# Kernel optimization log

Measured on AMD Instinct MI355X. Metric: run time of the kernel, lower is better.

Reference implementation:

```python
import jax, jax.numpy as jnp
import numpy as np

N_NODES = 10000
N_EDGES = 320000
F = 128
N_RBF = 20


def setup_inputs() -> dict:
    key = jax.random.key(0)
    ks = jax.random.split(key, 12)
    inp = {
        "idx_i": jax.random.randint(ks[0], (N_EDGES,), 0, N_NODES),
        "idx_j": jax.random.randint(ks[1], (N_EDGES,), 0, N_NODES),
        "rel_dir": jax.random.normal(ks[2], (N_EDGES, 3), dtype=jnp.float32),
        "rel_dist_cut": jax.random.uniform(ks[3], (N_EDGES,), dtype=jnp.float32),
        "rbf_features": jax.random.normal(ks[4], (N_EDGES, N_RBF), dtype=jnp.float32),
        "scalar_features": jax.random.normal(ks[5], (N_NODES, F), dtype=jnp.float32),
        "vector_features": jax.random.normal(ks[6], (N_NODES, F, 3), dtype=jnp.float32),
        # learned params: scalar_network = Linear(F,F) -> SiLU -> Linear(F,3F); rbf_network = Linear(N_RBF,3F)
        "W1": jax.random.normal(ks[7], (F, F), dtype=jnp.float32) / np.sqrt(F),
        "b1": jnp.zeros((F,), dtype=jnp.float32),
        "W2": jax.random.normal(ks[8], (F, 3 * F), dtype=jnp.float32) / np.sqrt(F),
        "b2": jnp.zeros((3 * F,), dtype=jnp.float32),
        "Wr": jax.random.normal(ks[9], (N_RBF, 3 * F), dtype=jnp.float32) / np.sqrt(N_RBF),
        "br": jnp.zeros((3 * F,), dtype=jnp.float32),
    }
    return inp


def reference(idx_i, idx_j, rel_dir, rel_dist_cut, rbf_features,
              scalar_features, vector_features, W1, b1, W2, b2, Wr, br):
    num_nodes, num_features = scalar_features.shape
    # per-node MLP: [N, 3F]
    phi = jax.nn.silu(scalar_features @ W1 + b1) @ W2 + b2
    # distance gate: [E, 3F]
    Wg = (rbf_features @ Wr + br) * rel_dist_cut[:, None]
    # gather neighbor phi and gate
    phi_W = phi[idx_j] * Wg                       # [E, 3F]
    phi_W_vv = phi_W[:, :num_features]            # [E, F]
    phi_W_ss = phi_W[:, num_features:2 * num_features]
    phi_W_vs = phi_W[:, 2 * num_features:]
    # per-receiver edge counts (bincount)
    counts = jax.ops.segment_sum(jnp.ones((idx_i.shape[0],), phi_W.dtype),
                                 idx_i, num_segments=num_nodes)  # [N]
    scalar_residuals = jax.ops.segment_sum(phi_W_ss, idx_i, num_segments=num_nodes)
    scalar_residuals = scalar_residuals / counts[:, None]
    # per-edge vector message: [E, F, 3]
    v_edge = (vector_features[idx_j] * phi_W_vv[:, :, None]
              + phi_W_vs[:, :, None] * rel_dir[:, None, :])
    vector_residuals = jax.ops.segment_sum(v_edge, idx_i, num_segments=num_nodes)
    vector_residuals = vector_residuals / counts[:, None, None]
    return (scalar_features + scalar_residuals,
            vector_features + vector_residuals)
```

## Files before the change

### kernel.cpp

```cpp
#include <hip/hip_runtime.h>
#include <hip/hip_bf16.h>

#define NN 10000
#define NE 320000
#define FDIM 128
#define NRBF 20
#define PHI_DIM 384
#define NKEY NN
#define SCAN_BLOCKS 40

typedef unsigned int uint;
typedef unsigned short ushort;

#if __has_builtin(__builtin_amdgcn_fdot2_f32_bf16)
#define USE_DOT2 1
typedef __bf16 bf16x2 __attribute__((ext_vector_type(2)));
#else
#define USE_DOT2 0
#endif

__device__ __forceinline__ ushort f2bf(float x) {
  __hip_bfloat16 b = __float2bfloat16(x);
  return *(ushort*)&b;
}


__global__ void phi_kernel(const float* __restrict__ S, const float* __restrict__ W1,
                           const float* __restrict__ b1, const float* __restrict__ W2,
                           const float* __restrict__ b2, const float* __restrict__ vf,
                           const int* __restrict__ idx_i, int* __restrict__ counts,
                           char* __restrict__ tab) {
  __shared__ float s_s[8][FDIM];
  __shared__ float h_s[8][FDIM];
  const int t = threadIdx.x;
  const int n0 = blockIdx.x * 8;
  {
    const int e0 = (blockIdx.x * 128 + t) * 2;
    atomicAdd(&counts[idx_i[e0]], 1);
    atomicAdd(&counts[idx_i[e0 + 1]], 1);
  }
  ushort vz[8];
#pragma unroll
  for (int n = 0; n < 8; n++) {
    const int node = n0 + n;
    const float* src = vf + (size_t)node * (FDIM * 3) + t * 3;
    char* pb = tab + (size_t)node * 1536;
    ((uint*)(pb + 1024))[t] = ((uint)f2bf(src[1]) << 16) | f2bf(src[0]);
    vz[n] = f2bf(src[2]);
  }
#pragma unroll
  for (int n = 0; n < 8; n++) s_s[n][t] = S[(n0 + n) * FDIM + t];
  __syncthreads();
  float acc[8];
#pragma unroll
  for (int n = 0; n < 8; n++) acc[n] = 0.f;
  for (int k = 0; k < FDIM; k++) {
    float w = W1[k * FDIM + t];
#pragma unroll
    for (int n = 0; n < 8; n++) acc[n] += s_s[n][k] * w;
  }
  float bb = b1[t];
#pragma unroll
  for (int n = 0; n < 8; n++) {
    float x = acc[n] + bb;
    h_s[n][t] = x / (1.0f + expf(-x));
  }
  __syncthreads();
  float a0[8], a1[8], a2[8];
#pragma unroll
  for (int n = 0; n < 8; n++) { a0[n] = 0.f; a1[n] = 0.f; a2[n] = 0.f; }
  for (int k = 0; k < FDIM; k++) {
    float w0 = W2[k * PHI_DIM + t];
    float w1 = W2[k * PHI_DIM + t + 128];
    float w2 = W2[k * PHI_DIM + t + 256];
#pragma unroll
    for (int n = 0; n < 8; n++) {
      float hv = h_s[n][k];
      a0[n] += hv * w0;
      a1[n] += hv * w1;
      a2[n] += hv * w2;
    }
  }
  float c0 = b2[t], c1 = b2[t + 128], c2 = b2[t + 256];
#pragma unroll
  for (int n = 0; n < 8; n++) {
    char* pb = tab + (size_t)(n0 + n) * 1536;
    ((uint*)pb)[t] = ((uint)f2bf(a1[n] + c1) << 16) | f2bf(a0[n] + c0);
    ((uint*)(pb + 512))[t] = ((uint)vz[n] << 16) | f2bf(a2[n] + c2);
  }
}

__global__ void scan1_kernel(const int* __restrict__ counts, int* __restrict__ offsets,
                             int* __restrict__ blocksums) {
  __shared__ int s[256];
  const int t = threadIdx.x;
  const int idx = blockIdx.x * 256 + t;
  const int c = counts[idx];
  s[t] = c;
  __syncthreads();
  for (int off = 1; off < 256; off <<= 1) {
    int v = (t >= off) ? s[t - off] : 0;
    __syncthreads();
    s[t] += v;
    __syncthreads();
  }
  if (idx < NKEY) offsets[idx] = s[t] - c;
  if (t == 255) blocksums[blockIdx.x] = s[255];
}

__global__ void scan2_kernel(int* __restrict__ blocksums, int* __restrict__ offsets) {
  __shared__ int s[64];
  const int t = threadIdx.x;
  int v0 = (t < SCAN_BLOCKS) ? blocksums[t] : 0;
  s[t] = v0;
  __syncthreads();
  for (int off = 1; off < 64; off <<= 1) {
    int v = (t >= off) ? s[t - off] : 0;
    __syncthreads();
    s[t] += v;
    __syncthreads();
  }
  if (t < SCAN_BLOCKS) blocksums[t] = s[t] - v0;
  if (t == SCAN_BLOCKS - 1) offsets[NKEY] = s[t];
}

__global__ void scan3_kernel(int* __restrict__ offsets, const int* __restrict__ blocksums) {
  const int idx = blockIdx.x * 256 + threadIdx.x;
  if (idx < NKEY) offsets[idx] += blocksums[blockIdx.x];
}

__global__ void stage_kernel(const int* __restrict__ idx_i, const int* __restrict__ idx_j,
                             const float* __restrict__ cut, const float* __restrict__ dir,
                             const float* __restrict__ rbf, const int* __restrict__ offsets,
                             int* __restrict__ cursor, uint* __restrict__ edata,
                             int* __restrict__ jlist) {
  int e = blockIdx.x * blockDim.x + threadIdx.x;
  if (e >= NE) return;
  int i = idx_i[e];
  int pos = atomicAdd(&cursor[i], 1);
  const int slot = offsets[i] + pos;
  const int j = idx_j[e];
  jlist[slot] = j;
  uint* d = edata + (size_t)slot * 16;
  const float c = cut[e];
  d[0] = (uint)j;
  d[1] = __float_as_uint(c);
  d[2] = __float_as_uint(dir[e * 3 + 0]);
  d[3] = __float_as_uint(dir[e * 3 + 1]);
  d[4] = __float_as_uint(dir[e * 3 + 2]);
  d[5] = 0u;
  const float* rb = rbf + (size_t)e * NRBF;
#pragma unroll
  for (int r = 0; r < 10; r++) {
    uint lo = (uint)f2bf(rb[2 * r] * c);
    uint hi = (uint)f2bf(rb[2 * r + 1] * c);
    d[6 + r] = (hi << 16) | lo;
  }
}

__global__ __launch_bounds__(128, 5) void node_kernel(
    const uint* __restrict__ edata, const int* __restrict__ jlist,
    const float* __restrict__ Wr, const float* __restrict__ br,
    const char* __restrict__ tab, const float* __restrict__ sf,
    const float* __restrict__ vf, const int* __restrict__ offsets,
    float* __restrict__ out) {
  const int f = threadIdx.x;
#if USE_DOT2
  bf16x2 wrA[10], wrB[10], wrC[10];
#pragma unroll
  for (int r = 0; r < 10; r++) {
    uint a = ((uint)f2bf(Wr[(2 * r + 1) * PHI_DIM + f]) << 16) | f2bf(Wr[(2 * r) * PHI_DIM + f]);
    uint b = ((uint)f2bf(Wr[(2 * r + 1) * PHI_DIM + f + 128]) << 16) |
             f2bf(Wr[(2 * r) * PHI_DIM + f + 128]);
    uint c = ((uint)f2bf(Wr[(2 * r + 1) * PHI_DIM + f + 256]) << 16) |
             f2bf(Wr[(2 * r) * PHI_DIM + f + 256]);
    wrA[r] = __builtin_bit_cast(bf16x2, a);
    wrB[r] = __builtin_bit_cast(bf16x2, b);
    wrC[r] = __builtin_bit_cast(bf16x2, c);
  }
#else
  float wrA[NRBF], wrB[NRBF], wrC[NRBF];
#pragma unroll
  for (int r = 0; r < NRBF; r++) {
    wrA[r] = Wr[r * PHI_DIM + f];
    wrB[r] = Wr[r * PHI_DIM + f + 128];
    wrC[r] = Wr[r * PHI_DIM + f + 256];
  }
#endif
  const int n = blockIdx.x;
  const int beg = offsets[n], end = offsets[n + 1];
  const float br0 = br[f], br1 = br[f + 128], br2 = br[f + 256];
  float ss = 0.f, ax = 0.f, ay = 0.f, az = 0.f;
  const int f4 = f * 4;

  auto process = [&](const uint4* rec, uint pq, uint zq, uint vq) {
    uint4 q0 = rec[0];
    uint4 q1 = rec[1];
    uint4 q2 = rec[2];
    uint4 q3 = rec[3];
    const float c = __uint_as_float(q0.y);
    const float dx = __uint_as_float(q0.z);
    const float dy = __uint_as_float(q0.w);
    const float dz = __uint_as_float(q1.x);
    uint rbp[10] = {q1.z, q1.w, q2.x, q2.y, q2.z, q2.w, q3.x, q3.y, q3.z, q3.w};
    float g0 = 0.f, g1 = 0.f, g2 = 0.f;
#if USE_DOT2
#pragma unroll
    for (int r = 0; r < 10; r++) {
      bf16x2 rp = __builtin_bit_cast(bf16x2, rbp[r]);
      g0 = __builtin_amdgcn_fdot2_f32_bf16(rp, wrA[r], g0, false);
      g1 = __builtin_amdgcn_fdot2_f32_bf16(rp, wrB[r], g1, false);
      g2 = __builtin_amdgcn_fdot2_f32_bf16(rp, wrC[r], g2, false);
    }
#else
#pragma unroll
    for (int r = 0; r < 10; r++) {
      float rlo = __uint_as_float(rbp[r] << 16);
      float rhi = __uint_as_float(rbp[r] & 0xffff0000u);
      g0 += rlo * wrA[2 * r] + rhi * wrA[2 * r + 1];
      g1 += rlo * wrB[2 * r] + rhi * wrB[2 * r + 1];
      g2 += rlo * wrC[2 * r] + rhi * wrC[2 * r + 1];
    }
#endif
    g0 += br0 * c;
    g1 += br1 * c;
    g2 += br2 * c;
    const float vv = __uint_as_float(pq << 16) * g0;
    const float sv = __uint_as_float(pq & 0xffff0000u) * g1;
    const float vs = __uint_as_float(zq << 16) * g2;
    ss += sv;
    ax += __uint_as_float(vq << 16) * vv + vs * dx;
    ay += __uint_as_float(vq & 0xffff0000u) * vv + vs * dy;
    az += __uint_as_float(zq & 0xffff0000u) * vv + vs * dz;
  };

  int p = beg;
  for (; p + 2 <= end; p += 2) {
    const int j0 = jlist[p];
    const int j1 = jlist[p + 1];
    const char* B0 = tab + (size_t)j0 * 1536;
    const char* B1 = tab + (size_t)j1 * 1536;
    const uint pq0 = *(const uint*)(B0 + f4);
    const uint zq0 = *(const uint*)(B0 + 512 + f4);
    const uint vq0 = *(const uint*)(B0 + 1024 + f4);
    const uint pq1 = *(const uint*)(B1 + f4);
    const uint zq1 = *(const uint*)(B1 + 512 + f4);
    const uint vq1 = *(const uint*)(B1 + 1024 + f4);
    const uint4* r0 = (const uint4*)(edata + (size_t)p * 16);
    const uint4* r1 = (const uint4*)(edata + (size_t)(p + 1) * 16);
    process(r0, pq0, zq0, vq0);
    process(r1, pq1, zq1, vq1);
  }
  if (p < end) {
    const int j0 = jlist[p];
    const char* B0 = tab + (size_t)j0 * 1536;
    const uint pq0 = *(const uint*)(B0 + f4);
    const uint zq0 = *(const uint*)(B0 + 512 + f4);
    const uint vq0 = *(const uint*)(B0 + 1024 + f4);
    process((const uint4*)(edata + (size_t)p * 16), pq0, zq0, vq0);
  }

  const float inv = 1.0f / (float)(end - beg);
  out[(size_t)n * FDIM + f] = sf[(size_t)n * FDIM + f] + ss * inv;
  float* ov = out + (size_t)NN * FDIM + (size_t)n * (FDIM * 3) + f * 3;
  const float* iv = vf + (size_t)n * (FDIM * 3) + f * 3;
  ov[0] = iv[0] + ax * inv;
  ov[1] = iv[1] + ay * inv;
  ov[2] = iv[2] + az * inv;
}

extern "C" void kernel_launch(void* const* d_in, const int* in_sizes, int n_in,
                              void* d_out, int out_size, void* d_ws, size_t ws_size,
                              hipStream_t stream) {
  const int* idx_i = (const int*)d_in[0];
  const int* idx_j = (const int*)d_in[1];
  const float* rel_dir = (const float*)d_in[2];
  const float* cut = (const float*)d_in[3];
  const float* rbf = (const float*)d_in[4];
  const float* sf = (const float*)d_in[5];
  const float* vf = (const float*)d_in[6];
  const float* W1 = (const float*)d_in[7];
  const float* b1 = (const float*)d_in[8];
  const float* W2 = (const float*)d_in[9];
  const float* b2 = (const float*)d_in[10];
  const float* Wr = (const float*)d_in[11];
  const float* br = (const float*)d_in[12];
  float* out = (float*)d_out;

  char* w = (char*)d_ws;
  int* counts = (int*)w;
  int* cursor = (int*)(w + 40960);
  int* offsets = (int*)(w + 81920);
  int* blocksums = (int*)(w + 122944);
  uint* edata = (uint*)(w + 123200);
  char* tab = w + 20603200;
  int* jlist = (int*)(w + 35963200);

  hipMemsetAsync(w, 0, 81920, stream);
  hipLaunchKernelGGL(phi_kernel, dim3(NN / 8), dim3(128), 0, stream, sf, W1, b1, W2, b2, vf,
                     idx_i, counts, tab);
  hipLaunchKernelGGL(scan1_kernel, dim3(SCAN_BLOCKS), dim3(256), 0, stream, counts, offsets,
                     blocksums);
  hipLaunchKernelGGL(scan2_kernel, dim3(1), dim3(64), 0, stream, blocksums, offsets);
  hipLaunchKernelGGL(scan3_kernel, dim3(SCAN_BLOCKS), dim3(256), 0, stream, offsets, blocksums);
  hipLaunchKernelGGL(stage_kernel, dim3((NE + 255) / 256), dim3(256), 0, stream, idx_i, idx_j,
                     cut, rel_dir, rbf, offsets, cursor, edata, jlist);
  hipLaunchKernelGGL(node_kernel, dim3(NN), dim3(128), 0, stream, edata, jlist, Wr, br, tab, sf,
                     vf, offsets, out);
}
```

Before: 165.6 us.

## Premultiply neighbor vectors by phi_vv per node and shrink gather table

The per-node table now stores vector_features times phi_vv (in bf16) instead of phi_vv and the raw vectors separately. This moves the multiply from the edge loop to the node kernel and shrinks each node's row from 1536 to 1280 bytes, cutting gather traffic in node_kernel. The stage kernel reuses the counts array as a decrementing cursor, which removes the separate cursor buffer and its memset. Rounding to bf16 now happens after the product rather than on each factor, which slightly changes numerics.

```diff
diff --git a/kernel.cpp b/kernel.cpp
--- a/kernel.cpp
+++ b/kernel.cpp
@@ -39,15 +39,6 @@
     atomicAdd(&counts[idx_i[e0]], 1);
     atomicAdd(&counts[idx_i[e0 + 1]], 1);
   }
-  ushort vz[8];
-#pragma unroll
-  for (int n = 0; n < 8; n++) {
-    const int node = n0 + n;
-    const float* src = vf + (size_t)node * (FDIM * 3) + t * 3;
-    char* pb = tab + (size_t)node * 1536;
-    ((uint*)(pb + 1024))[t] = ((uint)f2bf(src[1]) << 16) | f2bf(src[0]);
-    vz[n] = f2bf(src[2]);
-  }
 #pragma unroll
   for (int n = 0; n < 8; n++) s_s[n][t] = S[(n0 + n) * FDIM + t];
   __syncthreads();
@@ -84,9 +75,18 @@
   float c0 = b2[t], c1 = b2[t + 128], c2 = b2[t + 256];
 #pragma unroll
   for (int n = 0; n < 8; n++) {
-    char* pb = tab + (size_t)(n0 + n) * 1536;
-    ((uint*)pb)[t] = ((uint)f2bf(a1[n] + c1) << 16) | f2bf(a0[n] + c0);
-    ((uint*)(pb + 512))[t] = ((uint)vz[n] << 16) | f2bf(a2[n] + c2);
+    const int node = n0 + n;
+    const float p0 = a0[n] + c0;
+    const float p1 = a1[n] + c1;
+    const float p2 = a2[n] + c2;
+    const float* src = vf + (size_t)node * (FDIM * 3) + t * 3;
+    const uint wx = f2bf(src[0] * p0);
+    const uint wy = f2bf(src[1] * p0);
+    const uint wz = f2bf(src[2] * p0);
+    char* pb = tab + (size_t)node * 1280;
+    ((uint*)pb)[t] = (wy << 16) | wx;
+    ((uint*)(pb + 512))[t] = ((uint)f2bf(p1) << 16) | wz;
+    ((ushort*)(pb + 1024))[t] = f2bf(p2);
   }
 }
 
@@ -132,12 +132,12 @@
 __global__ void stage_kernel(const int* __restrict__ idx_i, const int* __restrict__ idx_j,
                              const float* __restrict__ cut, const float* __restrict__ dir,
                              const float* __restrict__ rbf, const int* __restrict__ offsets,
-                             int* __restrict__ cursor, uint* __restrict__ edata,
+                             int* __restrict__ counts, uint* __restrict__ edata,
                              int* __restrict__ jlist) {
   int e = blockIdx.x * blockDim.x + threadIdx.x;
   if (e >= NE) return;
   int i = idx_i[e];
-  int pos = atomicAdd(&cursor[i], 1);
+  int pos = atomicSub(&counts[i], 1) - 1;
   const int slot = offsets[i] + pos;
   const int j = idx_j[e];
   jlist[slot] = j;
@@ -193,7 +193,7 @@
   float ss = 0.f, ax = 0.f, ay = 0.f, az = 0.f;
   const int f4 = f * 4;
 
-  auto process = [&](const uint4* rec, uint pq, uint zq, uint vq) {
+  auto process = [&](const uint4* rec, uint d0, uint d1, uint zu) {
     uint4 q0 = rec[0];
     uint4 q1 = rec[1];
     uint4 q2 = rec[2];
@@ -225,39 +225,42 @@
     g0 += br0 * c;
     g1 += br1 * c;
     g2 += br2 * c;
-    const float vv = __uint_as_float(pq << 16) * g0;
-    const float sv = __uint_as_float(pq & 0xffff0000u) * g1;
-    const float vs = __uint_as_float(zq << 16) * g2;
-    ss += sv;
-    ax += __uint_as_float(vq << 16) * vv + vs * dx;
-    ay += __uint_as_float(vq & 0xffff0000u) * vv + vs * dy;
-    az += __uint_as_float(zq & 0xffff0000u) * vv + vs * dz;
+    const float wx = __uint_as_float(d0 << 16);
+    const float wy = __uint_as_float(d0 & 0xffff0000u);
+    const float wz = __uint_as_float(d1 << 16);
+    const float p1 = __uint_as_float(d1 & 0xffff0000u);
+    const float p2 = __uint_as_float(zu << 16);
+    const float vs = p2 * g2;
+    ss += p1 * g1;
+    ax += wx * g0 + vs * dx;
+    ay += wy * g0 + vs * dy;
+    az += wz * g0 + vs * dz;
   };
 
   int p = beg;
   for (; p + 2 <= end; p += 2) {
     const int j0 = jlist[p];
     const int j1 = jlist[p + 1];
-    const char* B0 = tab + (size_t)j0 * 1536;
-    const char* B1 = tab + (size_t)j1 * 1536;
-    const uint pq0 = *(const uint*)(B0 + f4);
-    const uint zq0 = *(const uint*)(B0 + 512 + f4);
-    const uint vq0 = *(const uint*)(B0 + 1024 + f4);
-    const uint pq1 = *(const uint*)(B1 + f4);
-    const uint zq1 = *(const uint*)(B1 + 512 + f4);
-    const uint vq1 = *(const uint*)(B1 + 1024 + f4);
+    const char* B0 = tab + (size_t)j0 * 1280;
+    const char* B1 = tab + (size_t)j1 * 1280;
+    const uint d00 = *(const uint*)(B0 + f4);
+    const uint d01 = *(const uint*)(B0 + 512 + f4);
+    const uint z0 = *(const ushort*)(B0 + 1024 + f * 2);
+    const uint d10 = *(const uint*)(B1 + f4);
+    const uint d11 = *(const uint*)(B1 + 512 + f4);
+    const uint z1 = *(const ushort*)(B1 + 1024 + f * 2);
     const uint4* r0 = (const uint4*)(edata + (size_t)p * 16);
     const uint4* r1 = (const uint4*)(edata + (size_t)(p + 1) * 16);
-    process(r0, pq0, zq0, vq0);
-    process(r1, pq1, zq1, vq1);
+    process(r0, d00, d01, z0);
+    process(r1, d10, d11, z1);
   }
   if (p < end) {
     const int j0 = jlist[p];
-    const char* B0 = tab + (size_t)j0 * 1536;
-    const uint pq0 = *(const uint*)(B0 + f4);
-    const uint zq0 = *(const uint*)(B0 + 512 + f4);
-    const uint vq0 = *(const uint*)(B0 + 1024 + f4);
-    process((const uint4*)(edata + (size_t)p * 16), pq0, zq0, vq0);
+    const char* B0 = tab + (size_t)j0 * 1280;
+    const uint d00 = *(const uint*)(B0 + f4);
+    const uint d01 = *(const uint*)(B0 + 512 + f4);
+    const uint z0 = *(const ushort*)(B0 + 1024 + f * 2);
+    process((const uint4*)(edata + (size_t)p * 16), d00, d01, z0);
   }
 
   const float inv = 1.0f / (float)(end - beg);
@@ -289,14 +292,13 @@
 
   char* w = (char*)d_ws;
   int* counts = (int*)w;
-  int* cursor = (int*)(w + 40960);
-  int* offsets = (int*)(w + 81920);
-  int* blocksums = (int*)(w + 122944);
-  uint* edata = (uint*)(w + 123200);
-  char* tab = w + 20603200;
-  int* jlist = (int*)(w + 35963200);
-
-  hipMemsetAsync(w, 0, 81920, stream);
+  int* offsets = (int*)(w + 40960);
+  int* blocksums = (int*)(w + 81920);
+  uint* edata = (uint*)(w + 90112);
+  char* tab = w + 20570112;
+  int* jlist = (int*)(w + 33370112);
+
+  hipMemsetAsync(w, 0, 40960, stream);
   hipLaunchKernelGGL(phi_kernel, dim3(NN / 8), dim3(128), 0, stream, sf, W1, b1, W2, b2, vf,
                      idx_i, counts, tab);
   hipLaunchKernelGGL(scan1_kernel, dim3(SCAN_BLOCKS), dim3(256), 0, stream, counts, offsets,
@@ -304,7 +306,7 @@
   hipLaunchKernelGGL(scan2_kernel, dim3(1), dim3(64), 0, stream, blocksums, offsets);
   hipLaunchKernelGGL(scan3_kernel, dim3(SCAN_BLOCKS), dim3(256), 0, stream, offsets, blocksums);
   hipLaunchKernelGGL(stage_kernel, dim3((NE + 255) / 256), dim3(256), 0, stream, idx_i, idx_j,
-                     cut, rel_dir, rbf, offsets, cursor, edata, jlist);
+                     cut, rel_dir, rbf, offsets, counts, edata, jlist);
   hipLaunchKernelGGL(node_kernel, dim3(NN), dim3(128), 0, stream, edata, jlist, Wr, br, tab, sf,
                      vf, offsets, out);
 }
```

Result: no change. 168.2 us (+1.6%).
